# Performance work log

Hardware: AMD Instinct MI355X
Metric: run time of the kernel (lower is better)

The kernel has to match this reference:

```python
import jax, jax.numpy as jnp
import numpy as np

EPS = 1e-8


def setup_inputs() -> dict:
    key = jax.random.key(0)
    k1, k2, k3 = jax.random.split(key, 3)
    n_nodes, n_pos, d, n_seg = 50000, 2048, 128, 32
    pred = jax.random.normal(k1, (n_nodes, d), dtype=jnp.float32)
    target = jax.random.normal(k2, (n_pos, d), dtype=jnp.float32)
    target_identifiers = jax.random.randint(k3, (n_pos,), 0, n_seg, dtype=jnp.int64)
    return {
        "pred": pred,
        "target": target,
        "target_identifiers": target_identifiers,
        "num_segments": n_seg,
    }


def reference(pred, target, target_identifiers, num_segments):
    # Pairwise L2 distance: sqrt(||t||^2 - 2 t.p + ||p||^2 + eps)
    # avoids materializing the [n_pos, n_nodes, d] broadcast tensor.
    t2 = jnp.sum(target * target, axis=-1, keepdims=True)          # [n_pos, 1]
    p2 = jnp.sum(pred * pred, axis=-1)                             # [n_nodes]
    cross = jnp.einsum('pd,nd->pn', target, pred)                  # [n_pos, n_nodes]
    sq = jnp.maximum(t2 - 2.0 * cross + p2[None, :], 0.0)
    dist_mat = jnp.sqrt(sq + EPS)                                  # [n_pos, n_nodes]

    # stage1: scatter_mean over target_identifiers (dim=0)
    seg_sum = jax.ops.segment_sum(dist_mat, target_identifiers,
                                  num_segments=num_segments)       # [n_seg, n_nodes]
    counts = jax.ops.segment_sum(jnp.ones((dist_mat.shape[0],), dist_mat.dtype),
                                 target_identifiers, num_segments=num_segments)
    seg_mean = seg_sum / jnp.maximum(counts, 1.0)[:, None]

    # stage2: mean over segments
    return seg_mean.mean(axis=0)                                   # [n_nodes]
```

## Files before the change

### kernel.cpp

```cpp
#include <hip/hip_runtime.h>

#define DIMK 128
#define POS_PER_BLOCK 512
#define NCHUNK 8
#define NODES_PER_BLOCK 128

typedef __bf16 bf16x8 __attribute__((ext_vector_type(8)));
typedef float  f32x4  __attribute__((ext_vector_type(4)));

__device__ inline unsigned short f32_to_bf16_rne(float f) {
    unsigned u = __float_as_uint(f);
    u += 0x7FFFu + ((u >> 16) & 1u);
    return (unsigned short)(u >> 16);
}


__global__ void pack_rows(const float* __restrict__ src,
                          unsigned short* __restrict__ dst,
                          float* __restrict__ norm2,
                          int n_valid, int n_rows_pad, float scale) {
    int wave = threadIdx.x >> 6, lane = threadIdx.x & 63;
    int row = blockIdx.x * 4 + wave;
    if (row >= n_rows_pad) return;
    int srow = min(row, n_valid - 1);
    int e = lane * 2;
    float2 v = *(const float2*)(src + (size_t)srow * DIMK + e);
    unsigned pk = (unsigned)f32_to_bf16_rne(scale * v.x) |
                  ((unsigned)f32_to_bf16_rne(scale * v.y) << 16);
    int tile = row >> 4, col = row & 15;
    int kk = e >> 5, kb = (e >> 3) & 3, j = e & 7;
    size_t off = (size_t)tile * 2048 + kk * 512 + (kb * 16 + col) * 8 + j;
    *(unsigned*)(dst + off) = pk;
    float s = v.x * v.x + v.y * v.y;
#pragma unroll
    for (int o = 1; o < 64; o <<= 1) s += __shfl_xor(s, o, 64);
    if (lane == 0) norm2[row] = s;
}

__global__ void seg_weights(const int* __restrict__ ids,
                            const int* __restrict__ nseg_p,
                            float* __restrict__ wsa, int n_pos) {
    __shared__ int   cnt[256];
    __shared__ float w[256];
    int nseg = nseg_p[0];
    if (nseg > 256) nseg = 256;
    int t = threadIdx.x;
    if (t < nseg) cnt[t] = 0;
    __syncthreads();
    for (int p = t; p < n_pos; p += blockDim.x) atomicAdd(&cnt[ids[p]], 1);
    __syncthreads();
    if (t < nseg) w[t] = 1.0f / ((float)nseg * (float)max(cnt[t], 1));
    __syncthreads();
    for (int p = t; p < n_pos; p += blockDim.x) wsa[p] = w[ids[p]];
}

__global__ __launch_bounds__(256, 4)
void l2dist_main(const unsigned short* __restrict__ pb,
                 const float* __restrict__ p2,
                 const unsigned short* __restrict__ tb,
                 const float* __restrict__ t2g,
                 const float* __restrict__ wg,
                 float* __restrict__ out,
                 int n_nodes) {
    __shared__ __align__(16) unsigned short lbuf[2][8192];
    __shared__ __align__(16) float t2_lds[POS_PER_BLOCK];
    __shared__ __align__(16) float w_lds[POS_PER_BLOCK];

    const int tid  = threadIdx.x;
    const int lane = tid & 63;
    const int wave = tid >> 6;
    const int col  = lane & 15;
    const int kb   = lane >> 4;
    const int n0   = blockIdx.y * NODES_PER_BLOCK + wave * 32;
    const int tbase = blockIdx.x * (POS_PER_BLOCK / 16);
    const int rbase = blockIdx.x * POS_PER_BLOCK;

    bf16x8 bfrag[2][4];
    float p2g[2];
    const unsigned short* bp = pb + ((size_t)(n0 >> 4)) * 2048 + (size_t)lane * 8;
#pragma unroll
    for (int g = 0; g < 2; ++g) {
#pragma unroll
        for (int kk = 0; kk < 4; ++kk)
            bfrag[g][kk] = *(const bf16x8*)(bp + g * 2048 + kk * 512);
        p2g[g] = p2[n0 + g * 16 + col];
    }

    t2_lds[tid]       = t2g[rbase + tid];
    t2_lds[tid + 256] = t2g[rbase + tid + 256];
    w_lds[tid]        = wg[rbase + tid];
    w_lds[tid + 256]  = wg[rbase + tid + 256];

    const unsigned short* sgp = tb + (size_t)tbase * 2048 + wave * 512 + lane * 8;
#define STAGE(C)                                                               \
    _Pragma("unroll")                                                          \
    for (int t_ = 0; t_ < 4; ++t_) {                                           \
        __builtin_amdgcn_global_load_lds(                                      \
            (const __attribute__((address_space(1))) unsigned int*)(const void*)\
                (sgp + (size_t)((C) * 4 + t_) * 2048),                         \
            (__attribute__((address_space(3))) unsigned int*)(void*)           \
                (&lbuf[(C) & 1][t_ * 2048] + wave * 512),                      \
            16, 0, 0);                                                         \
    }

    STAGE(0);
    STAGE(1);

    asm volatile("s_waitcnt lgkmcnt(0)" ::: "memory");
    __builtin_amdgcn_s_barrier();

    float acc0 = 0.f, acc1 = 0.f;

#pragma unroll
    for (int c = 0; c < NCHUNK; ++c) {
        if (c < NCHUNK - 1) { asm volatile("s_waitcnt vmcnt(4)" ::: "memory"); }
        else                { asm volatile("s_waitcnt vmcnt(0)" ::: "memory"); }
        __builtin_amdgcn_s_barrier();

        __builtin_amdgcn_s_setprio(1);
#pragma unroll
        for (int t = 0; t < 4; ++t) {
            const unsigned short* rb = &lbuf[c & 1][t * 2048] + lane * 8;
            bf16x8 a0 = *(const bf16x8*)(rb);
            bf16x8 a1 = *(const bf16x8*)(rb + 512);
            bf16x8 a2 = *(const bf16x8*)(rb + 1024);
            bf16x8 a3 = *(const bf16x8*)(rb + 1536);

            int pr = (c * 4 + t) * 16 + kb * 4;
            f32x4 t2v = *(const f32x4*)&t2_lds[pr];
            f32x4 wv  = *(const f32x4*)&w_lds[pr];

            f32x4 d0 = t2v + p2g[0];
            f32x4 d1 = t2v + p2g[1];
            d0 = __builtin_amdgcn_mfma_f32_16x16x32_bf16(a0, bfrag[0][0], d0, 0, 0, 0);
            d1 = __builtin_amdgcn_mfma_f32_16x16x32_bf16(a0, bfrag[1][0], d1, 0, 0, 0);
            d0 = __builtin_amdgcn_mfma_f32_16x16x32_bf16(a1, bfrag[0][1], d0, 0, 0, 0);
            d1 = __builtin_amdgcn_mfma_f32_16x16x32_bf16(a1, bfrag[1][1], d1, 0, 0, 0);
            d0 = __builtin_amdgcn_mfma_f32_16x16x32_bf16(a2, bfrag[0][2], d0, 0, 0, 0);
            d1 = __builtin_amdgcn_mfma_f32_16x16x32_bf16(a2, bfrag[1][2], d1, 0, 0, 0);
            d0 = __builtin_amdgcn_mfma_f32_16x16x32_bf16(a3, bfrag[0][3], d0, 0, 0, 0);
            d1 = __builtin_amdgcn_mfma_f32_16x16x32_bf16(a3, bfrag[1][3], d1, 0, 0, 0);

#pragma unroll
            for (int j = 0; j < 4; ++j) {
                acc0 = fmaf(wv[j], __builtin_amdgcn_sqrtf(fmaxf(d0[j], 0.f)), acc0);
                acc1 = fmaf(wv[j], __builtin_amdgcn_sqrtf(fmaxf(d1[j], 0.f)), acc1);
            }
        }
        __builtin_amdgcn_s_setprio(0);

        if (c + 2 < NCHUNK) {
            __builtin_amdgcn_s_barrier();
            STAGE(c + 2);
        }
    }
#undef STAGE

    acc0 += __shfl_xor(acc0, 16, 64);  acc0 += __shfl_xor(acc0, 32, 64);
    acc1 += __shfl_xor(acc1, 16, 64);  acc1 += __shfl_xor(acc1, 32, 64);
    if (lane < 16) {
        int na = n0 + col;
        if (na      < n_nodes) atomicAdd(out + na,      acc0);
        if (na + 16 < n_nodes) atomicAdd(out + na + 16, acc1);
    }
}

extern "C" void kernel_launch(void* const* d_in, const int* in_sizes, int n_in,
                              void* d_out, int out_size, void* d_ws, size_t ws_size,
                              hipStream_t stream) {
    const float* pred  = (const float*)d_in[0];
    const float* tgt   = (const float*)d_in[1];
    const int*   ids   = (const int*)d_in[2];
    const int*   nsegp = (const int*)d_in[3];
    float* out = (float*)d_out;

    int n_nodes = in_sizes[0] / DIMK;
    int n_pos   = in_sizes[2];

    int gy = (n_nodes + NODES_PER_BLOCK - 1) / NODES_PER_BLOCK;
    int n_rows_pad = gy * NODES_PER_BLOCK;

    char* ws = (char*)d_ws;
    size_t off_pb = 0;
    size_t off_tb = off_pb + (size_t)n_rows_pad * DIMK * 2;
    size_t off_p2 = off_tb + (size_t)n_pos * DIMK * 2;
    size_t off_t2 = off_p2 + (size_t)n_rows_pad * 4;
    size_t off_w  = off_t2 + (size_t)n_pos * 4;
    unsigned short* pb  = (unsigned short*)(ws + off_pb);
    unsigned short* tb  = (unsigned short*)(ws + off_tb);
    float*          p2  = (float*)(ws + off_p2);
    float*          t2  = (float*)(ws + off_t2);
    float*          wsa = (float*)(ws + off_w);

    pack_rows<<<(n_rows_pad + 3) / 4, 256, 0, stream>>>(pred, pb, p2, n_nodes, n_rows_pad, 1.0f);
    pack_rows<<<(n_pos + 3) / 4, 256, 0, stream>>>(tgt, tb, t2, n_pos, n_pos, -2.0f);
    seg_weights<<<1, 1024, 0, stream>>>(ids, nsegp, wsa, n_pos);
    hipMemsetAsync(out, 0, (size_t)out_size * sizeof(float), stream);

    dim3 grid(n_pos / POS_PER_BLOCK, gy);
    l2dist_main<<<grid, 256, 0, stream>>>(pb, p2, tb, t2, wsa, out, n_nodes);
}
```

Before: 57.22 us.

## Double nodes per wave and swap MFMA operands so positions map to columns

Each wave now covers 64 nodes instead of 32, so every target fragment read from LDS feeds twice as many MFMAs, and each block covers 256 nodes. The MFMA operands are swapped so nodes sit on output rows and positions on columns. The per-position t2 and weight become one scalar per lane, and p2 loads as a vector. The final reduction becomes a 4-step butterfly over 16 lanes per accumulator, with more atomics per thread. The cost is higher register pressure (16 fragments, 16 accumulators) that may hurt occupancy at launch_bounds(256,4), plus a longer epilogue.

```diff
diff --git a/kernel.cpp b/kernel.cpp
--- a/kernel.cpp
+++ b/kernel.cpp
@@ -3,7 +3,7 @@
 #define DIMK 128
 #define POS_PER_BLOCK 512
 #define NCHUNK 8
-#define NODES_PER_BLOCK 128
+#define NODES_PER_BLOCK 256
 
 typedef __bf16 bf16x8 __attribute__((ext_vector_type(8)));
 typedef float  f32x4  __attribute__((ext_vector_type(4)));
@@ -71,19 +71,19 @@
     const int wave = tid >> 6;
     const int col  = lane & 15;
     const int kb   = lane >> 4;
-    const int n0   = blockIdx.y * NODES_PER_BLOCK + wave * 32;
+    const int n0   = blockIdx.y * NODES_PER_BLOCK + wave * 64;
     const int tbase = blockIdx.x * (POS_PER_BLOCK / 16);
     const int rbase = blockIdx.x * POS_PER_BLOCK;
 
-    bf16x8 bfrag[2][4];
-    float p2g[2];
+    bf16x8 pfrag[4][4];
+    f32x4  p2r[4];
     const unsigned short* bp = pb + ((size_t)(n0 >> 4)) * 2048 + (size_t)lane * 8;
 #pragma unroll
-    for (int g = 0; g < 2; ++g) {
+    for (int g = 0; g < 4; ++g) {
 #pragma unroll
         for (int kk = 0; kk < 4; ++kk)
-            bfrag[g][kk] = *(const bf16x8*)(bp + g * 2048 + kk * 512);
-        p2g[g] = p2[n0 + g * 16 + col];
+            pfrag[g][kk] = *(const bf16x8*)(bp + g * 2048 + kk * 512);
+        p2r[g] = *(const f32x4*)(p2 + n0 + g * 16 + kb * 4);
     }
 
     t2_lds[tid]       = t2g[rbase + tid];
@@ -109,7 +109,8 @@
     asm volatile("s_waitcnt lgkmcnt(0)" ::: "memory");
     __builtin_amdgcn_s_barrier();
 
-    float acc0 = 0.f, acc1 = 0.f;
+    f32x4 acc0 = {0.f,0.f,0.f,0.f}, acc1 = {0.f,0.f,0.f,0.f};
+    f32x4 acc2 = {0.f,0.f,0.f,0.f}, acc3 = {0.f,0.f,0.f,0.f};
 
 #pragma unroll
     for (int c = 0; c < NCHUNK; ++c) {
@@ -126,25 +127,38 @@
             bf16x8 a2 = *(const bf16x8*)(rb + 1024);
             bf16x8 a3 = *(const bf16x8*)(rb + 1536);
 
-            int pr = (c * 4 + t) * 16 + kb * 4;
-            f32x4 t2v = *(const f32x4*)&t2_lds[pr];
-            f32x4 wv  = *(const f32x4*)&w_lds[pr];
-
-            f32x4 d0 = t2v + p2g[0];
-            f32x4 d1 = t2v + p2g[1];
-            d0 = __builtin_amdgcn_mfma_f32_16x16x32_bf16(a0, bfrag[0][0], d0, 0, 0, 0);
-            d1 = __builtin_amdgcn_mfma_f32_16x16x32_bf16(a0, bfrag[1][0], d1, 0, 0, 0);
-            d0 = __builtin_amdgcn_mfma_f32_16x16x32_bf16(a1, bfrag[0][1], d0, 0, 0, 0);
-            d1 = __builtin_amdgcn_mfma_f32_16x16x32_bf16(a1, bfrag[1][1], d1, 0, 0, 0);
-            d0 = __builtin_amdgcn_mfma_f32_16x16x32_bf16(a2, bfrag[0][2], d0, 0, 0, 0);
-            d1 = __builtin_amdgcn_mfma_f32_16x16x32_bf16(a2, bfrag[1][2], d1, 0, 0, 0);
-            d0 = __builtin_amdgcn_mfma_f32_16x16x32_bf16(a3, bfrag[0][3], d0, 0, 0, 0);
-            d1 = __builtin_amdgcn_mfma_f32_16x16x32_bf16(a3, bfrag[1][3], d1, 0, 0, 0);
+            int pr = (c * 4 + t) * 16 + col;
+            float t2c = t2_lds[pr];
+            float wc  = w_lds[pr];
+
+            f32x4 d0 = p2r[0] + t2c;
+            f32x4 d1 = p2r[1] + t2c;
+            d0 = __builtin_amdgcn_mfma_f32_16x16x32_bf16(pfrag[0][0], a0, d0, 0, 0, 0);
+            d1 = __builtin_amdgcn_mfma_f32_16x16x32_bf16(pfrag[1][0], a0, d1, 0, 0, 0);
+            d0 = __builtin_amdgcn_mfma_f32_16x16x32_bf16(pfrag[0][1], a1, d0, 0, 0, 0);
+            d1 = __builtin_amdgcn_mfma_f32_16x16x32_bf16(pfrag[1][1], a1, d1, 0, 0, 0);
+            d0 = __builtin_amdgcn_mfma_f32_16x16x32_bf16(pfrag[0][2], a2, d0, 0, 0, 0);
+            d1 = __builtin_amdgcn_mfma_f32_16x16x32_bf16(pfrag[1][2], a2, d1, 0, 0, 0);
+            d0 = __builtin_amdgcn_mfma_f32_16x16x32_bf16(pfrag[0][3], a3, d0, 0, 0, 0);
+            d1 = __builtin_amdgcn_mfma_f32_16x16x32_bf16(pfrag[1][3], a3, d1, 0, 0, 0);
+
+            f32x4 e0 = p2r[2] + t2c;
+            f32x4 e1 = p2r[3] + t2c;
+            e0 = __builtin_amdgcn_mfma_f32_16x16x32_bf16(pfrag[2][0], a0, e0, 0, 0, 0);
+            e1 = __builtin_amdgcn_mfma_f32_16x16x32_bf16(pfrag[3][0], a0, e1, 0, 0, 0);
+            e0 = __builtin_amdgcn_mfma_f32_16x16x32_bf16(pfrag[2][1], a1, e0, 0, 0, 0);
+            e1 = __builtin_amdgcn_mfma_f32_16x16x32_bf16(pfrag[3][1], a1, e1, 0, 0, 0);
+            e0 = __builtin_amdgcn_mfma_f32_16x16x32_bf16(pfrag[2][2], a2, e0, 0, 0, 0);
+            e1 = __builtin_amdgcn_mfma_f32_16x16x32_bf16(pfrag[3][2], a2, e1, 0, 0, 0);
+            e0 = __builtin_amdgcn_mfma_f32_16x16x32_bf16(pfrag[2][3], a3, e0, 0, 0, 0);
+            e1 = __builtin_amdgcn_mfma_f32_16x16x32_bf16(pfrag[3][3], a3, e1, 0, 0, 0);
 
 #pragma unroll
             for (int j = 0; j < 4; ++j) {
-                acc0 = fmaf(wv[j], __builtin_amdgcn_sqrtf(fmaxf(d0[j], 0.f)), acc0);
-                acc1 = fmaf(wv[j], __builtin_amdgcn_sqrtf(fmaxf(d1[j], 0.f)), acc1);
+                acc0[j] = fmaf(wc, __builtin_amdgcn_sqrtf(fmaxf(d0[j], 0.f)), acc0[j]);
+                acc1[j] = fmaf(wc, __builtin_amdgcn_sqrtf(fmaxf(d1[j], 0.f)), acc1[j]);
+                acc2[j] = fmaf(wc, __builtin_amdgcn_sqrtf(fmaxf(e0[j], 0.f)), acc2[j]);
+                acc3[j] = fmaf(wc, __builtin_amdgcn_sqrtf(fmaxf(e1[j], 0.f)), acc3[j]);
             }
         }
         __builtin_amdgcn_s_setprio(0);
@@ -156,12 +170,25 @@
     }
 #undef STAGE
 
-    acc0 += __shfl_xor(acc0, 16, 64);  acc0 += __shfl_xor(acc0, 32, 64);
-    acc1 += __shfl_xor(acc1, 16, 64);  acc1 += __shfl_xor(acc1, 32, 64);
-    if (lane < 16) {
-        int na = n0 + col;
-        if (na      < n_nodes) atomicAdd(out + na,      acc0);
-        if (na + 16 < n_nodes) atomicAdd(out + na + 16, acc1);
+#pragma unroll
+    for (int m = 1; m <= 8; m <<= 1) {
+#pragma unroll
+        for (int j = 0; j < 4; ++j) {
+            acc0[j] += __shfl_xor(acc0[j], m, 64);
+            acc1[j] += __shfl_xor(acc1[j], m, 64);
+            acc2[j] += __shfl_xor(acc2[j], m, 64);
+            acc3[j] += __shfl_xor(acc3[j], m, 64);
+        }
+    }
+    if (col == 0) {
+        int nb = n0 + kb * 4;
+#pragma unroll
+        for (int j = 0; j < 4; ++j) {
+            if (nb + j      < n_nodes) atomicAdd(out + nb + j,      acc0[j]);
+            if (nb + 16 + j < n_nodes) atomicAdd(out + nb + 16 + j, acc1[j]);
+            if (nb + 32 + j < n_nodes) atomicAdd(out + nb + 32 + j, acc2[j]);
+            if (nb + 48 + j < n_nodes) atomicAdd(out + nb + 48 + j, acc3[j]);
+        }
     }
 }
 
```

Result: slower. 148.3 us (+159.1%).
